# Performance work log

Hardware: AMD Instinct MI355X
Metric: run time of the kernel (lower is better)

The kernel has to match this reference:

```python
import jax, jax.numpy as jnp
import numpy as np

B, S, D = 8, 2048, 1024


def setup_inputs() -> dict:
    key = jax.random.key(0)
    k1, k2, k3, k4, k5 = jax.random.split(key, 5)
    scale = 1.0 / np.sqrt(D)
    x = jax.random.normal(k1, (B, S, D), dtype=jnp.float32)
    Wq = jax.random.normal(k2, (D, D), dtype=jnp.float32) * scale
    Wk = jax.random.normal(k3, (D, D), dtype=jnp.float32) * scale
    Wv = jax.random.normal(k4, (D, D), dtype=jnp.float32) * scale
    # sequence lengths in [1, S]
    lens = jax.random.randint(k5, (B,), 1, S + 1, dtype=jnp.int32)
    return {"x": x, "lens": lens, "Wq": Wq, "Wk": Wk, "Wv": Wv}


def reference(x, lens, Wq, Wk, Wv):
    # nn.Linear(bias=False): y = x @ W.T
    q = jnp.einsum('bsd,ed->bse', x, Wq)
    k = jnp.einsum('bsd,ed->bse', x, Wk)
    v = jnp.einsum('bsd,ed->bse', x, Wv)
    # scores: QK^T / sqrt(D)  -> [B, S, S]
    scores = jnp.einsum('bqd,bkd->bqk', q, k) / jnp.sqrt(jnp.asarray(D, x.dtype))
    # key-padding mask from lens: True where key position >= len (masked to -inf)
    key_pad = jnp.arange(S)[None, :] >= lens[:, None]          # [B, S]
    scores = jnp.where(key_pad[:, None, :], -jnp.inf, scores)  # broadcast over query dim
    att = jax.nn.softmax(scores, axis=2)
    return jnp.einsum('bqk,bkd->bqd', att, v)
```

## Files before the change

kernel.cpp:

```cpp
#include <hip/hip_runtime.h>
#include <stdint.h>

typedef __bf16 bf16;
typedef __bf16 bf16x8 __attribute__((ext_vector_type(8)));
typedef __bf16 bf16x4 __attribute__((ext_vector_type(4)));
typedef float f32x4 __attribute__((ext_vector_type(4)));
typedef float f32x16 __attribute__((ext_vector_type(16)));

#define DEV static __device__ __forceinline__

DEV void async_copy16(const bf16* gsrc, const bf16* ldst) {
  __builtin_amdgcn_global_load_lds(
      (__attribute__((address_space(1))) void*)(uintptr_t)gsrc,
      (__attribute__((address_space(3))) void*)(uint32_t)(uintptr_t)ldst,
      16, 0, 0);
}

DEV void gemm_tile32(const bf16* __restrict__ A, const bf16* __restrict__ B,
                     int lda, int ldb, int kTiles,
                     bf16* As, bf16* Bs, f32x16 acc[2][2]) {
  const int tid  = threadIdx.x;
  const int wave = tid >> 6;
  const int lane = tid & 63;
  const int wm = (wave >> 1) * 64;
  const int wn = (wave & 1) * 64;
  const int rf = lane & 31;
  const int kh = (lane >> 5) * 8;
  const int sw = (lane & 7) * 8;

  const int srow = tid >> 3;
  const int scol = ((tid & 7) ^ (srow & 7)) * 8;
  const bf16* Ag = A + (size_t)srow * lda + scol;
  const bf16* Bg = B + (size_t)srow * ldb + scol;
  bf16* Asw = As + wave * 512;
  bf16* Bsw = Bs + wave * 512;

  for (int kt = 0; kt < kTiles; ++kt) {
    __syncthreads();
    const bf16* ag = Ag + kt * 64;
    const bf16* bg = Bg + kt * 64;
#pragma unroll
    for (int i = 0; i < 4; ++i) {
      async_copy16(ag + (size_t)(i * 32) * lda, Asw + i * 2048);
      async_copy16(bg + (size_t)(i * 32) * ldb, Bsw + i * 2048);
    }
    __syncthreads();
#pragma unroll
    for (int ks = 0; ks < 4; ++ks) {
      const int off = (ks * 16 + kh) ^ sw;
      bf16x8 a0 = *(const bf16x8*)&As[(wm + rf) * 64 + off];
      bf16x8 a1 = *(const bf16x8*)&As[(wm + 32 + rf) * 64 + off];
      bf16x8 b0 = *(const bf16x8*)&Bs[(wn + rf) * 64 + off];
      bf16x8 b1 = *(const bf16x8*)&Bs[(wn + 32 + rf) * 64 + off];
      acc[0][0] = __builtin_amdgcn_mfma_f32_32x32x16_bf16(a0, b0, acc[0][0], 0, 0, 0);
      acc[0][1] = __builtin_amdgcn_mfma_f32_32x32x16_bf16(a0, b1, acc[0][1], 0, 0, 0);
      acc[1][0] = __builtin_amdgcn_mfma_f32_32x32x16_bf16(a1, b0, acc[1][0], 0, 0, 0);
      acc[1][1] = __builtin_amdgcn_mfma_f32_32x32x16_bf16(a1, b1, acc[1][1], 0, 0, 0);
    }
  }
}

#define EPILOGUE32(STMT)                                                     \
  do {                                                                       \
    const int lane = threadIdx.x & 63, wave = threadIdx.x >> 6;              \
    const int colb = n0 + (wave & 1) * 64 + (lane & 31);                     \
    const int rowb = m0 + (wave >> 1) * 64 + (lane >> 5) * 4;                \
    _Pragma("unroll") for (int i = 0; i < 2; ++i)                            \
      _Pragma("unroll") for (int reg = 0; reg < 16; ++reg) {                 \
        size_t row = rowb + i * 32 + (reg & 3) + 8 * (reg >> 2);             \
        _Pragma("unroll") for (int j = 0; j < 2; ++j) {                      \
          size_t col = colb + j * 32;                                        \
          float val = acc[i][j][reg];                                        \
          STMT;                                                              \
        }                                                                    \
      }                                                                      \
  } while (0)

__global__ __launch_bounds__(256) void k_cast_all(const float* __restrict__ X,
                                                  const float* __restrict__ Wq,
                                                  const float* __restrict__ Wk,
                                                  const float* __restrict__ Wv,
                                                  bf16* __restrict__ Xb,
                                                  bf16* __restrict__ Wb) {
  int i = blockIdx.x * 256 + threadIdx.x;
  const float* src;
  bf16* dst;
  int off;
  if (i < 4194304) {
    src = X; dst = Xb; off = i;
  } else {
    int j = i - 4194304;
    int which = j >> 18;
    src = (which == 0) ? Wq : ((which == 1) ? Wk : Wv);
    dst = Wb + (size_t)(j >> 18) * 1048576;
    off = j & 262143;
  }
  float4 v = ((const float4*)src)[off];
  bf16x4 o = {(bf16)v.x, (bf16)v.y, (bf16)v.z, (bf16)v.w};
  ((bf16x4*)dst)[off] = o;
}

__global__ __launch_bounds__(512, 2) void k_gemm_qkv(
    const bf16* __restrict__ X, const bf16* __restrict__ W,
    const int* __restrict__ lens, bf16* __restrict__ QKV) {
  const int n0 = blockIdx.x * 256;
  const int m0 = blockIdx.y * 256;
  if (n0 >= 1024 && (m0 & 2047) >= lens[m0 >> 11]) return;
  __shared__ __align__(16) char smem[65536];

  const int tid = threadIdx.x;
  const int lane = tid & 63, wid = tid >> 6;

  int grow0, gcol0, grow1, gcol1;
  {
    int g = tid, rho = g >> 3, sig = (g & 7) ^ (rho & 7);
    grow0 = 2 * rho + (sig >> 2); gcol0 = (sig & 3) * 8;
    g = tid + 512; rho = g >> 3; sig = (g & 7) ^ (rho & 7);
    grow1 = 2 * rho + (sig >> 2); gcol1 = (sig & 3) * 8;
  }
  const bf16* pa0 = X + (size_t)(m0 + grow0) * 1024 + gcol0;
  const bf16* pa1 = X + (size_t)(m0 + grow1) * 1024 + gcol1;
  const bf16* pb0 = W + (size_t)(n0 + grow0) * 1024 + gcol0;
  const bf16* pb1 = W + (size_t)(n0 + grow1) * 1024 + gcol1;

#define QKV_STAGE(kt, slot)                                  \
  do {                                                       \
    const int ko_ = (kt) * 32;                               \
    char* sb_ = smem + (slot) * 32768 + wid * 1024;          \
    async_copy16(pa0 + ko_, (const bf16*)sb_);               \
    async_copy16(pa1 + ko_, (const bf16*)(sb_ + 8192));      \
    async_copy16(pb0 + ko_, (const bf16*)(sb_ + 16384));     \
    async_copy16(pb1 + ko_, (const bf16*)(sb_ + 24576));     \
  } while (0)

  const int mf = lane & 15, jb = lane >> 4;
  const int wm = (wid >> 2) * 128, wn = (wid & 3) * 64;
  const uint32_t pbyte = (uint32_t)((((((mf & 1) << 2) | jb) ^ ((mf >> 1) & 7))) * 16);
  const uint32_t laneA = (uint32_t)(wm * 64 + (mf >> 1) * 128) + pbyte;
  const uint32_t laneB = 16384u + (uint32_t)(wn * 64 + (mf >> 1) * 128) + pbyte;

  f32x4 acc[8][4] = {};

  QKV_STAGE(0, 0);
  QKV_STAGE(1, 1);
  asm volatile("s_waitcnt vmcnt(4)" ::: "memory");
  __builtin_amdgcn_sched_barrier(0);
  __builtin_amdgcn_s_barrier();
  __builtin_amdgcn_sched_barrier(0);

  for (int t = 0; t < 32; ++t) {
    const char* As = smem + (t & 1) * 32768 + laneA;
    const char* Bs = smem + (t & 1) * 32768 + laneB;
    bf16x8 af[8], bfr[4];
#pragma unroll
    for (int i = 0; i < 8; ++i) af[i] = *(const bf16x8*)(As + i * 1024);
#pragma unroll
    for (int j = 0; j < 4; ++j) bfr[j] = *(const bf16x8*)(Bs + j * 1024);
    __builtin_amdgcn_s_setprio(1);
#pragma unroll
    for (int i = 0; i < 8; ++i)
#pragma unroll
      for (int j = 0; j < 4; ++j)
        acc[i][j] = __builtin_amdgcn_mfma_f32_16x16x32_bf16(af[i], bfr[j], acc[i][j], 0, 0, 0);
    __builtin_amdgcn_s_setprio(0);
    asm volatile("s_waitcnt lgkmcnt(0)" ::: "memory");
    __builtin_amdgcn_sched_barrier(0);
    __builtin_amdgcn_s_barrier();
    __builtin_amdgcn_sched_barrier(0);
    const int nx = (t + 2 < 32) ? t + 2 : 31;
    QKV_STAGE(nx, t & 1);
    asm volatile("s_waitcnt vmcnt(4)" ::: "memory");
    __builtin_amdgcn_sched_barrier(0);
    __builtin_amdgcn_s_barrier();
    __builtin_amdgcn_sched_barrier(0);
  }
#undef QKV_STAGE

  const float qscale = (n0 < 1024) ? 0.03125f : 1.0f;
  const int colb = n0 + wn + mf;
  const int rowb = m0 + wm + jb * 4;
#pragma unroll
  for (int i = 0; i < 8; ++i)
#pragma unroll
    for (int r = 0; r < 4; ++r) {
      bf16* dst = QKV + (size_t)(rowb + i * 16 + r) * 3072 + colb;
#pragma unroll
      for (int j = 0; j < 4; ++j) dst[j * 16] = (bf16)(acc[i][j][r] * qscale);
    }
}

__global__ __launch_bounds__(256) void k_transpose_v(const bf16* __restrict__ QKV,
                                                     const int* __restrict__ lens,
                                                     bf16* __restrict__ Vt) {
  __shared__ bf16 tile[32][33];
  const int b = blockIdx.z;
  const int s0 = blockIdx.x * 32;
  if (s0 >= ((lens[b] + 63) & ~63)) return;
  const int d0 = blockIdx.y * 32;
  const int tx = threadIdx.x, ty = threadIdx.y;
#pragma unroll
  for (int i = 0; i < 4; ++i)
    tile[ty + i * 8][tx] = QKV[(size_t)(b * 2048 + s0 + ty + i * 8) * 3072 + 2048 + d0 + tx];
  __syncthreads();
#pragma unroll
  for (int i = 0; i < 4; ++i)
    Vt[(size_t)(b * 1024 + d0 + ty + i * 8) * 2048 + s0 + tx] = tile[tx][ty + i * 8];
}

__global__ __launch_bounds__(256) void k_gemm_scores(const bf16* __restrict__ QKV,
                                                     const int* __restrict__ lens,
                                                     bf16* __restrict__ S) {
  const int b = blockIdx.z;
  const int len = lens[b];
  const int n0 = blockIdx.x * 128;
  if (n0 >= len) return;
  const int m0 = blockIdx.y * 128;
  __shared__ __align__(16) bf16 As[128 * 64];
  __shared__ __align__(16) bf16 Bs[128 * 64];
  const bf16* Q = QKV + (size_t)b * 2048 * 3072;
  const bf16* K = Q + 1024;
  f32x16 acc[2][2] = {};
  gemm_tile32(Q + (size_t)m0 * 3072, K + (size_t)n0 * 3072, 3072, 3072, 16, As, Bs, acc);
  bf16* Sb = S + (size_t)b * 2048 * 2048;
  EPILOGUE32(Sb[row * 2048 + col] = (bf16)val);
}

__global__ __launch_bounds__(256) void k_softmax(bf16* __restrict__ S,
                                                 const int* __restrict__ lens) {
  const int row = blockIdx.x;
  const int len = lens[row >> 11];
  const int kmax = (len + 63) & ~63;
  bf16* Sr = S + (size_t)row * 2048;
  const int tid = threadIdx.x;
  const int base = tid * 8;
  __shared__ float red[4];

  float f[8];
  if (base < len) {
    bf16x8 v = ((const bf16x8*)Sr)[tid];
#pragma unroll
    for (int e = 0; e < 8; ++e) f[e] = (base + e < len) ? (float)v[e] : -1e30f;
  } else {
#pragma unroll
    for (int e = 0; e < 8; ++e) f[e] = -1e30f;
  }
  float m = -1e30f;
#pragma unroll
  for (int e = 0; e < 8; ++e) m = fmaxf(m, f[e]);
#pragma unroll
  for (int off = 32; off; off >>= 1) m = fmaxf(m, __shfl_xor(m, off));
  if ((tid & 63) == 0) red[tid >> 6] = m;
  __syncthreads();
  m = fmaxf(fmaxf(red[0], red[1]), fmaxf(red[2], red[3]));
  __syncthreads();

  float s = 0.f;
#pragma unroll
  for (int e = 0; e < 8; ++e) {
    float p = (base + e < len) ? __expf(f[e] - m) : 0.f;
    f[e] = p;
    s += p;
  }
#pragma unroll
  for (int off = 32; off; off >>= 1) s += __shfl_xor(s, off);
  if ((tid & 63) == 0) red[tid >> 6] = s;
  __syncthreads();
  s = red[0] + red[1] + red[2] + red[3];
  const float inv = 1.f / s;

  if (base < kmax) {
    bf16x8 o;
#pragma unroll
    for (int e = 0; e < 8; ++e) o[e] = (bf16)(f[e] * inv);
    ((bf16x8*)Sr)[tid] = o;
  }
}

__global__ __launch_bounds__(256) void k_gemm_out(const bf16* __restrict__ P,
                                                  const bf16* __restrict__ Vt,
                                                  const int* __restrict__ lens,
                                                  float* __restrict__ Out) {
  const int b = blockIdx.z;
  const int kTiles = (lens[b] + 63) >> 6;
  const int n0 = blockIdx.x * 128;
  const int m0 = blockIdx.y * 128;
  __shared__ __align__(16) bf16 As[128 * 64];
  __shared__ __align__(16) bf16 Bs[128 * 64];
  const bf16* Pb = P + (size_t)b * 2048 * 2048;
  const bf16* Vb = Vt + (size_t)b * 1024 * 2048;
  f32x16 acc[2][2] = {};
  gemm_tile32(Pb + (size_t)m0 * 2048, Vb + (size_t)n0 * 2048, 2048, 2048, kTiles, As, Bs, acc);
  float* Ob = Out + (size_t)b * 2048 * 1024;
  EPILOGUE32(Ob[row * 1024 + col] = val);
}

extern "C" void kernel_launch(void* const* d_in, const int* in_sizes, int n_in,
                              void* d_out, int out_size, void* d_ws, size_t ws_size,
                              hipStream_t stream) {
  const float* x   = (const float*)d_in[0];
  const int* lens  = (const int*)d_in[1];
  const float* Wq  = (const float*)d_in[2];
  const float* Wk  = (const float*)d_in[3];
  const float* Wv  = (const float*)d_in[4];
  float* out = (float*)d_out;

  char* ws = (char*)d_ws;
  bf16* S   = (bf16*)(ws);
  bf16* Xb  = (bf16*)(ws);
  bf16* Wb  = (bf16*)(ws + 33554432);
  bf16* QKV = (bf16*)(ws + 67108864);
  bf16* Vt  = (bf16*)(ws + 167772160);

  k_cast_all<<<19456, 256, 0, stream>>>(x, Wq, Wk, Wv, Xb, Wb);
  k_gemm_qkv<<<dim3(12, 64), 512, 0, stream>>>(Xb, Wb, lens, QKV);
  k_transpose_v<<<dim3(64, 32, 8), dim3(32, 8), 0, stream>>>(QKV, lens, Vt);
  k_gemm_scores<<<dim3(16, 16, 8), 256, 0, stream>>>(QKV, lens, S);
  k_softmax<<<16384, 256, 0, stream>>>(S, lens);
  k_gemm_out<<<dim3(8, 16, 8), 256, 0, stream>>>(S, Vt, lens, out);
}
```

Baseline: 385.9 us.

## Restructure QKV GEMM into 4-phase interleaved pipeline with K=64 stages and block swizzle

Rewrites the QKV projection GEMM main loop to use 64-wide K stages in a 128KB double buffer, splitting each iteration into four MFMA quadrants. Each quadrant's LDS fragment loads and global-to-LDS async copies are interleaved with the MFMAs of another quadrant. The 2D grid becomes a 1D grid with an XCD-aware swizzle of block indices, meant to improve L2 reuse across chiplets. The goal is to hide load latency and cut barrier stalls, at the cost of more LDS per block, which may reduce occupancy, and more complex waitcnt bookkeeping.

```diff
diff --git a/kernel.cpp b/kernel.cpp
--- a/kernel.cpp
+++ b/kernel.cpp
@@ -8,12 +8,17 @@
 typedef float f32x16 __attribute__((ext_vector_type(16)));
 
 #define DEV static __device__ __forceinline__
+#define SB0() __builtin_amdgcn_sched_barrier(0)
 
 DEV void async_copy16(const bf16* gsrc, const bf16* ldst) {
   __builtin_amdgcn_global_load_lds(
       (__attribute__((address_space(1))) void*)(uintptr_t)gsrc,
       (__attribute__((address_space(3))) void*)(uint32_t)(uintptr_t)ldst,
       16, 0, 0);
+}
+
+DEV f32x4 MF(bf16x8 a, bf16x8 b, f32x4 c) {
+  return __builtin_amdgcn_mfma_f32_16x16x32_bf16(a, b, c, 0, 0, 0);
 }
 
 DEV void gemm_tile32(const bf16* __restrict__ A, const bf16* __restrict__ B,
@@ -103,87 +108,160 @@
 __global__ __launch_bounds__(512, 2) void k_gemm_qkv(
     const bf16* __restrict__ X, const bf16* __restrict__ W,
     const int* __restrict__ lens, bf16* __restrict__ QKV) {
-  const int n0 = blockIdx.x * 256;
-  const int m0 = blockIdx.y * 256;
+  const int bid = blockIdx.x;
+  const int swz = (bid & 7) * 96 + (bid >> 3);
+  const int m_blk = swz / 12;
+  const int n_blk = swz - m_blk * 12;
+  const int m0 = m_blk << 8, n0 = n_blk << 8;
   if (n0 >= 1024 && (m0 & 2047) >= lens[m0 >> 11]) return;
-  __shared__ __align__(16) char smem[65536];
+
+  __shared__ __align__(16) char smem[131072];
+  const char* smemc = (const char*)smem;
 
   const int tid = threadIdx.x;
   const int lane = tid & 63, wid = tid >> 6;
-
-  int grow0, gcol0, grow1, gcol1;
-  {
-    int g = tid, rho = g >> 3, sig = (g & 7) ^ (rho & 7);
-    grow0 = 2 * rho + (sig >> 2); gcol0 = (sig & 3) * 8;
-    g = tid + 512; rho = g >> 3; sig = (g & 7) ^ (rho & 7);
-    grow1 = 2 * rho + (sig >> 2); gcol1 = (sig & 3) * 8;
-  }
-  const bf16* pa0 = X + (size_t)(m0 + grow0) * 1024 + gcol0;
-  const bf16* pa1 = X + (size_t)(m0 + grow1) * 1024 + gcol1;
-  const bf16* pb0 = W + (size_t)(n0 + grow0) * 1024 + gcol0;
-  const bf16* pb1 = W + (size_t)(n0 + grow1) * 1024 + gcol1;
-
-#define QKV_STAGE(kt, slot)                                  \
-  do {                                                       \
-    const int ko_ = (kt) * 32;                               \
-    char* sb_ = smem + (slot) * 32768 + wid * 1024;          \
-    async_copy16(pa0 + ko_, (const bf16*)sb_);               \
-    async_copy16(pa1 + ko_, (const bf16*)(sb_ + 8192));      \
-    async_copy16(pb0 + ko_, (const bf16*)(sb_ + 16384));     \
-    async_copy16(pb1 + ko_, (const bf16*)(sb_ + 24576));     \
-  } while (0)
-
   const int mf = lane & 15, jb = lane >> 4;
   const int wm = (wid >> 2) * 128, wn = (wid & 3) * 64;
-  const uint32_t pbyte = (uint32_t)((((((mf & 1) << 2) | jb) ^ ((mf >> 1) & 7))) * 16);
-  const uint32_t laneA = (uint32_t)(wm * 64 + (mf >> 1) * 128) + pbyte;
-  const uint32_t laneB = 16384u + (uint32_t)(wn * 64 + (mf >> 1) * 128) + pbyte;
-
+
+  const uint32_t pbyte = (uint32_t)(((((mf & 1) << 2) | jb) ^ ((mf >> 1) & 7)) * 16);
+  const uint32_t rbase = (uint32_t)((mf >> 1) * 128) + pbyte;
+#define LDA(i, ks, bof) (*(const bf16x8*)(smemc + (bof) + (ks) * 16384 + wm * 64 + (i) * 1024 + rbase))
+#define LDB(j, ks, bof) (*(const bf16x8*)(smemc + (bof) + 32768 + (ks) * 16384 + wn * 64 + (j) * 1024 + rbase))
+
+  const int sig = (tid & 7) ^ ((tid >> 3) & 7);
+  const int rowbase = 2 * (tid >> 3) + (sig >> 2);
+  const int colb = (sig & 3) * 8;
+  const bf16* gA = X + (size_t)(m0 + rowbase) * 1024 + colb;
+  const bf16* gB = W + (size_t)(n0 + rowbase) * 1024 + colb;
+
+#define STG(gp, region, h, kt, P)                                          \
+  do {                                                                     \
+    const bf16* s_ = (gp) + (size_t)(h) * 131072 + (size_t)(kt) * 64;      \
+    char* d_ = smem + (size_t)(P) * 65536 + (region) + (h) * 8192 + wid * 1024; \
+    async_copy16(s_,      (const bf16*)d_);                                \
+    async_copy16(s_ + 32, (const bf16*)(d_ + 16384));                      \
+  } while (0)
+
+  bf16x8 af[4][2], blo[2][2], bhi[2][2];
   f32x4 acc[8][4] = {};
 
-  QKV_STAGE(0, 0);
-  QKV_STAGE(1, 1);
-  asm volatile("s_waitcnt vmcnt(4)" ::: "memory");
-  __builtin_amdgcn_sched_barrier(0);
+  STG(gA, 0,     0, 0, 0);
+  STG(gB, 32768, 0, 0, 0);
+  STG(gB, 32768, 1, 0, 0);
+  STG(gA, 0,     1, 0, 0);
+  STG(gB, 32768, 0, 1, 1);
+  STG(gA, 0,     0, 1, 1);
+  STG(gB, 32768, 1, 1, 1);
+  asm volatile("s_waitcnt vmcnt(6)" ::: "memory");
+  SB0();
   __builtin_amdgcn_s_barrier();
-  __builtin_amdgcn_sched_barrier(0);
-
-  for (int t = 0; t < 32; ++t) {
-    const char* As = smem + (t & 1) * 32768 + laneA;
-    const char* Bs = smem + (t & 1) * 32768 + laneB;
-    bf16x8 af[8], bfr[4];
-#pragma unroll
-    for (int i = 0; i < 8; ++i) af[i] = *(const bf16x8*)(As + i * 1024);
-#pragma unroll
-    for (int j = 0; j < 4; ++j) bfr[j] = *(const bf16x8*)(Bs + j * 1024);
+  SB0();
+
+#pragma unroll 2
+  for (int t = 0; t < 16; ++t) {
+    const uint32_t bof = (uint32_t)(t & 1) << 16;
+    const int P = t & 1;
+
+#pragma unroll
+    for (int i = 0; i < 4; ++i) { af[i][0] = LDA(i, 0, bof); af[i][1] = LDA(i, 1, bof); }
+#pragma unroll
+    for (int j = 0; j < 2; ++j) { blo[j][0] = LDB(j, 0, bof); blo[j][1] = LDB(j, 1, bof); }
+    if (t <= 14) STG(gA, 0, 1, t + 1, P ^ 1);
+    asm volatile("s_waitcnt lgkmcnt(8)" ::: "memory");
+    SB0();
+    __builtin_amdgcn_s_barrier();
+    asm volatile("s_waitcnt lgkmcnt(0)" ::: "memory");
+    SB0();
     __builtin_amdgcn_s_setprio(1);
 #pragma unroll
-    for (int i = 0; i < 8; ++i)
-#pragma unroll
-      for (int j = 0; j < 4; ++j)
-        acc[i][j] = __builtin_amdgcn_mfma_f32_16x16x32_bf16(af[i], bfr[j], acc[i][j], 0, 0, 0);
+    for (int i = 0; i < 4; ++i)
+#pragma unroll
+      for (int j = 0; j < 2; ++j) {
+        acc[i][j] = MF(af[i][0], blo[j][0], acc[i][j]);
+        acc[i][j] = MF(af[i][1], blo[j][1], acc[i][j]);
+      }
     __builtin_amdgcn_s_setprio(0);
+    SB0();
+    __builtin_amdgcn_s_barrier();
+    SB0();
+
+#pragma unroll
+    for (int j = 0; j < 2; ++j) { bhi[j][0] = LDB(j + 2, 0, bof); bhi[j][1] = LDB(j + 2, 1, bof); }
+    SB0();
+    __builtin_amdgcn_s_barrier();
     asm volatile("s_waitcnt lgkmcnt(0)" ::: "memory");
-    __builtin_amdgcn_sched_barrier(0);
-    __builtin_amdgcn_s_barrier();
-    __builtin_amdgcn_sched_barrier(0);
-    const int nx = (t + 2 < 32) ? t + 2 : 31;
-    QKV_STAGE(nx, t & 1);
-    asm volatile("s_waitcnt vmcnt(4)" ::: "memory");
-    __builtin_amdgcn_sched_barrier(0);
-    __builtin_amdgcn_s_barrier();
-    __builtin_amdgcn_sched_barrier(0);
-  }
-#undef QKV_STAGE
+    SB0();
+    __builtin_amdgcn_s_setprio(1);
+#pragma unroll
+    for (int i = 0; i < 4; ++i)
+#pragma unroll
+      for (int j = 0; j < 2; ++j) {
+        acc[i][j + 2] = MF(af[i][0], bhi[j][0], acc[i][j + 2]);
+        acc[i][j + 2] = MF(af[i][1], bhi[j][1], acc[i][j + 2]);
+      }
+    __builtin_amdgcn_s_setprio(0);
+    SB0();
+    __builtin_amdgcn_s_barrier();
+    SB0();
+
+#pragma unroll
+    for (int i = 0; i < 4; ++i) { af[i][0] = LDA(i + 4, 0, bof); af[i][1] = LDA(i + 4, 1, bof); }
+    if (t <= 13) STG(gB, 32768, 0, t + 2, P);
+    SB0();
+    __builtin_amdgcn_s_barrier();
+    asm volatile("s_waitcnt lgkmcnt(0)" ::: "memory");
+    SB0();
+    __builtin_amdgcn_s_setprio(1);
+#pragma unroll
+    for (int i = 0; i < 4; ++i)
+#pragma unroll
+      for (int j = 0; j < 2; ++j) {
+        acc[i + 4][j + 2] = MF(af[i][0], bhi[j][0], acc[i + 4][j + 2]);
+        acc[i + 4][j + 2] = MF(af[i][1], bhi[j][1], acc[i + 4][j + 2]);
+      }
+    __builtin_amdgcn_s_setprio(0);
+    SB0();
+    __builtin_amdgcn_s_barrier();
+    SB0();
+
+    if (t <= 13) {
+      STG(gA, 0,     0, t + 2, P);
+      STG(gB, 32768, 1, t + 2, P);
+    }
+    SB0();
+    __builtin_amdgcn_s_setprio(1);
+#pragma unroll
+    for (int i = 0; i < 4; ++i)
+#pragma unroll
+      for (int j = 0; j < 2; ++j) {
+        acc[i + 4][j] = MF(af[i][0], blo[j][0], acc[i + 4][j]);
+        acc[i + 4][j] = MF(af[i][1], blo[j][1], acc[i + 4][j]);
+      }
+    __builtin_amdgcn_s_setprio(0);
+    SB0();
+    if (t <= 13) {
+      asm volatile("s_waitcnt vmcnt(6)" ::: "memory");
+    } else if (t == 14) {
+      asm volatile("s_waitcnt vmcnt(0)" ::: "memory");
+    }
+    if (t < 15) {
+      SB0();
+      __builtin_amdgcn_s_barrier();
+      SB0();
+    }
+  }
+#undef STG
+#undef LDA
+#undef LDB
 
   const float qscale = (n0 < 1024) ? 0.03125f : 1.0f;
-  const int colb = n0 + wn + mf;
-  const int rowb = m0 + wm + jb * 4;
+  const int colw = n0 + wn + mf;
+  const int roww = m0 + wm + jb * 4;
 #pragma unroll
   for (int i = 0; i < 8; ++i)
 #pragma unroll
     for (int r = 0; r < 4; ++r) {
-      bf16* dst = QKV + (size_t)(rowb + i * 16 + r) * 3072 + colb;
+      bf16* dst = QKV + (size_t)(roww + i * 16 + r) * 3072 + colw;
 #pragma unroll
       for (int j = 0; j < 4; ++j) dst[j * 16] = (bf16)(acc[i][j][r] * qscale);
     }
@@ -312,7 +390,7 @@
   bf16* Vt  = (bf16*)(ws + 167772160);
 
   k_cast_all<<<19456, 256, 0, stream>>>(x, Wq, Wk, Wv, Xb, Wb);
-  k_gemm_qkv<<<dim3(12, 64), 512, 0, stream>>>(Xb, Wb, lens, QKV);
+  k_gemm_qkv<<<768, 512, 0, stream>>>(Xb, Wb, lens, QKV);
   k_transpose_v<<<dim3(64, 32, 8), dim3(32, 8), 0, stream>>>(QKV, lens, Vt);
   k_gemm_scores<<<dim3(16, 16, 8), 256, 0, stream>>>(QKV, lens, S);
   k_softmax<<<16384, 256, 0, stream>>>(S, lens);
```

New measurement: 376.1 us. -2.5%, faster.
